# Optimization experiments

Hardware: AMD Instinct MI355X
Metric: run time of the kernel (lower is better)

## Reference

```python
import jax, jax.numpy as jnp
import numpy as np

N_NODES = 50000
N_EDGES = 1600000
IN_SIZE = 256
HIDDEN = 16
HEADS = 8
OUT_SIZE = 16
NEG_SLOPE = 0.2


def setup_inputs() -> dict:
    key = jax.random.key(0)
    ks = jax.random.split(key, 12)
    node_feat = jax.random.normal(ks[0], (N_NODES, IN_SIZE), dtype=jnp.float32)
    src = jax.random.randint(ks[1], (N_EDGES,), 0, N_NODES)
    dst = jax.random.randint(ks[2], (N_EDGES,), 0, N_NODES)
    d1 = HEADS * HIDDEN  # 128
    W1 = jax.random.normal(ks[3], (IN_SIZE, d1), dtype=jnp.float32) / np.sqrt(IN_SIZE)
    al1 = jax.random.normal(ks[4], (HEADS, HIDDEN), dtype=jnp.float32) / np.sqrt(HIDDEN)
    ar1 = jax.random.normal(ks[5], (HEADS, HIDDEN), dtype=jnp.float32) / np.sqrt(HIDDEN)
    b1 = jnp.zeros((d1,), dtype=jnp.float32)
    W2 = jax.random.normal(ks[6], (d1, HEADS * OUT_SIZE), dtype=jnp.float32) / np.sqrt(d1)
    al2 = jax.random.normal(ks[7], (HEADS, OUT_SIZE), dtype=jnp.float32) / np.sqrt(OUT_SIZE)
    ar2 = jax.random.normal(ks[8], (HEADS, OUT_SIZE), dtype=jnp.float32) / np.sqrt(OUT_SIZE)
    b2 = jnp.zeros((HEADS * OUT_SIZE,), dtype=jnp.float32)
    return {"node_feat": node_feat, "src": src, "dst": dst,
            "W1": W1, "al1": al1, "ar1": ar1, "b1": b1,
            "W2": W2, "al2": al2, "ar2": ar2, "b2": b2}


def _gat_conv(h, src, dst, W, attn_l, attn_r, bias, num_nodes):
    """DGL GATConv (eval mode, no dropout, no residual). Returns [N, H, D]."""
    H, D = attn_l.shape
    feat = (h @ W).reshape(-1, H, D)            # [N, H, D]
    el = jnp.sum(feat * attn_l, axis=-1)         # [N, H]
    er = jnp.sum(feat * attn_r, axis=-1)         # [N, H]
    e = jax.nn.leaky_relu(el[src] + er[dst], NEG_SLOPE)   # [E, H]
    # segment softmax over incoming edges of each dst node
    m = jax.ops.segment_max(e, dst, num_segments=num_nodes)
    m = jnp.where(jnp.isfinite(m), m, 0.0)       # guard isolated nodes
    ex = jnp.exp(e - m[dst])
    denom = jax.ops.segment_sum(ex, dst, num_segments=num_nodes)
    alpha = ex / denom[dst]                      # [E, H]
    msg = alpha[:, :, None] * feat[src]          # [E, H, D]
    out = jax.ops.segment_sum(msg, dst, num_segments=num_nodes)  # [N, H, D]
    return out + bias.reshape(H, D)


def reference(node_feat, src, dst, W1, al1, ar1, b1, W2, al2, ar2, b2):
    h = _gat_conv(node_feat, src, dst, W1, al1, ar1, b1, N_NODES)
    h = jax.nn.elu(h).reshape(N_NODES, -1)       # flatten(1) after activation
    out = _gat_conv(h, src, dst, W2, al2, ar2, b2, N_NODES)
    return out.mean(axis=1)                      # mean over heads -> [N, out_size]
```

## Files before the change

kernel.cpp:

```cpp
#include <hip/hip_runtime.h>
#include <hip/hip_bf16.h>

#define N_NODES 50000
#define N_EDGES 1600000
#define HEADS 8
#define HDIM 16
#define D1 128
#define NEG_SLOPE 0.2f
#define RTILES 3125
#define NB 196
#define BCAP 12288
#define B1BLK 320
#define EPB1 5000
#define WPREP_BLKS 217
#define GEMM_BLKS 782
#define B2BLK 392
#define B2CAP 8192

typedef short short8 __attribute__((ext_vector_type(8)));
typedef float f32x4 __attribute__((ext_vector_type(4)));
typedef _Float16 half8 __attribute__((ext_vector_type(8)));
typedef unsigned char uchar;

__device__ __forceinline__ float bf2f(ushort u) {
    union { unsigned u; float f; } x; x.u = ((unsigned)u) << 16; return x.f;
}
__device__ __forceinline__ ushort f2bf(float f) {
    union { float f; unsigned u; } x; x.f = f;
    unsigned r = x.u + 0x7FFF + ((x.u >> 16) & 1);
    return (ushort)(r >> 16);
}
__device__ __forceinline__ float ldf(const void* p, size_t i, int isf32) {
    return isf32 ? ((const float*)p)[i] : bf2f(((const ushort*)p)[i]);
}
__device__ __forceinline__ void splitbf(float f, ushort& hi, ushort& lo) {
    unsigned u = __float_as_uint(f);
    unsigned uh = u & 0xFFFF0000u;
    hi = (ushort)(uh >> 16);
    lo = f2bf(f - __uint_as_float(uh));
}

#define O_ROWPTR   0
#define O_GCUR     200064
#define O_FLAGS    602240
#define O_ESRC     2202624
#define O_W1HI     5402624
#define O_W1LO     5476352
#define O_W2HI     5550080
#define O_W2LO     5586944
#define O_B1F      5623808
#define O_B2F      5624320
#define O_FEATG    5624832
#define O_EL       18424832
#define O_ER       20024832
#define O_FEATG2   21624832
#define O_EL2      34424832
#define O_ER2      36024832
#define O_PKBUF    O_FEATG2


__global__ __launch_bounds__(256) void k_detect(const ushort* __restrict__ w1, int* __restrict__ flags,
                                                int* __restrict__ gcur) {
    __shared__ int sm[256];
    int t = threadIdx.x;
    if (blockIdx.x == 1) {
        if (t < NB) gcur[t] = 0;
        return;
    }
    int cnt = 0;
    for (int i = t; i < 32768; i += 256) {
        int e = (w1[i] >> 7) & 0xFF;
        if (e >= 0xC8) cnt++;
    }
    sm[t] = cnt; __syncthreads();
    for (int off = 128; off > 0; off >>= 1) {
        if (t < off) sm[t] += sm[t + off];
        __syncthreads();
    }
    if (t == 0) flags[0] = (sm[0] > 0) ? 1 : 0;
}

__device__ __forceinline__ void wprep_elem(const void* W, const void* al, const void* ar,
                                           int K, int kshift, ushort* whi, ushort* wlo,
                                           int isf32, int idx) {
    if (idx >= 144 * K) return;
    int n = idx >> kshift, k = idx & (K - 1);
    float f;
    if (n < 128) {
        f = ldf(W, (size_t)k * 128 + n, isf32);
    } else if (n < 136) {
        int h = n - 128;
        f = 0.f;
#pragma unroll
        for (int d = 0; d < HDIM; ++d)
            f = fmaf(ldf(W, (size_t)k * 128 + h * 16 + d, isf32), ldf(al, h * 16 + d, isf32), f);
    } else {
        int h = n - 136;
        f = 0.f;
#pragma unroll
        for (int d = 0; d < HDIM; ++d)
            f = fmaf(ldf(W, (size_t)k * 128 + h * 16 + d, isf32), ldf(ar, h * 16 + d, isf32), f);
    }
    ushort hi = f2bf(f);
    wlo[n * K + k] = f2bf(f - bf2f(hi));
    whi[n * K + k] = hi;
}

__device__ __forceinline__ void block_scan(int* sm, int t) {
    for (int off = 1; off < 256; off <<= 1) {
        int v = (t >= off) ? sm[t - off] : 0;
        __syncthreads();
        sm[t] += v;
        __syncthreads();
    }
}

#define B1_SMEM 28384

__global__ __launch_bounds__(256) void k_wb1(const void* __restrict__ W1, const void* __restrict__ al1,
                                             const void* __restrict__ ar1, const void* __restrict__ b1,
                                             const void* __restrict__ W2, const void* __restrict__ al2,
                                             const void* __restrict__ ar2, const void* __restrict__ b2,
                                             ushort* __restrict__ w1hi, ushort* __restrict__ w1lo,
                                             ushort* __restrict__ w2hi, ushort* __restrict__ w2lo,
                                             float* __restrict__ b1f, float* __restrict__ b2f,
                                             const int4* __restrict__ src4, const int4* __restrict__ dst4,
                                             int* __restrict__ gcur, uint* __restrict__ pkbuf,
                                             const int* __restrict__ flags) {
    __shared__ __align__(16) char smem[B1_SMEM];
    int b = blockIdx.x, t = threadIdx.x;
    if (b < WPREP_BLKS) {
        int isf32 = flags[0];
        if (b < 144) {
            wprep_elem(W1, al1, ar1, 256, 8, w1hi, w1lo, isf32, b * 256 + t);
        } else if (b < 216) {
            wprep_elem(W2, al2, ar2, 128, 7, w2hi, w2lo, isf32, (b - 144) * 256 + t);
        } else {
            if (t < 128) b1f[t] = ldf(b1, t, isf32);
            else b2f[t - 128] = ldf(b2, t - 128, isf32);
        }
    } else {
        uint*  stage = (uint*)smem;
        uchar* bid   = (uchar*)(smem + 20000);
        uint*  cnt   = (uint*)(smem + 25000);
        int*   loff  = (int*)(smem + 25784);
        int*   goff  = (int*)(smem + 26568);
        int*   sm    = (int*)(smem + 27352);
        int bb = b - WPREP_BLKS;
        for (int w = t; w < NB; w += 256) cnt[w] = 0;
        __syncthreads();
        int base4 = bb * (EPB1 / 4);
        for (int g = t; g < EPB1 / 4; g += 256) {
            int4 d = dst4[base4 + g];
            atomicAdd(&cnt[d.x >> 8], 1u);
            atomicAdd(&cnt[d.y >> 8], 1u);
            atomicAdd(&cnt[d.z >> 8], 1u);
            atomicAdd(&cnt[d.w >> 8], 1u);
        }
        __syncthreads();
        int c = (t < NB) ? (int)cnt[t] : 0;
        sm[t] = c;
        __syncthreads();
        block_scan(sm, t);
        if (t < NB) {
            loff[t] = sm[t] - c;
            goff[t] = atomicAdd(&gcur[t], c);
            cnt[t] = 0;
        }
        __syncthreads();
        for (int g = t; g < EPB1 / 4; g += 256) {
            int4 s = src4[base4 + g];
            int4 d = dst4[base4 + g];
            { int bk = d.x >> 8; int r = atomicAdd(&cnt[bk], 1u); int p = loff[bk] + r; stage[p] = ((uint)s.x << 8) | (uint)(d.x & 255); bid[p] = (uchar)bk; }
            { int bk = d.y >> 8; int r = atomicAdd(&cnt[bk], 1u); int p = loff[bk] + r; stage[p] = ((uint)s.y << 8) | (uint)(d.y & 255); bid[p] = (uchar)bk; }
            { int bk = d.z >> 8; int r = atomicAdd(&cnt[bk], 1u); int p = loff[bk] + r; stage[p] = ((uint)s.z << 8) | (uint)(d.z & 255); bid[p] = (uchar)bk; }
            { int bk = d.w >> 8; int r = atomicAdd(&cnt[bk], 1u); int p = loff[bk] + r; stage[p] = ((uint)s.w << 8) | (uint)(d.w & 255); bid[p] = (uchar)bk; }
        }
        __syncthreads();
        for (int k = t; k < EPB1; k += 256) {
            int bk = (int)bid[k];
            int gi = goff[bk] + (k - loff[bk]);
            if (gi < BCAP) pkbuf[(size_t)bk * BCAP + gi] = stage[k];
        }
    }
}

__device__ __forceinline__ void store_tile(_Float16 (*sfe)[72], _Float16* featg,
                                           const f32x4* acc, int lane, int quad, int l16,
                                           int rowb0, int cbase) {
#pragma unroll
    for (int ci = 0; ci < 4; ++ci)
#pragma unroll
        for (int r = 0; r < 4; ++r)
            sfe[quad * 4 + r][ci * 16 + l16] = (_Float16)acc[ci][r];
    int rr = lane >> 3, ch = lane & 7;
#pragma unroll
    for (int s = 0; s < 2; ++s) {
        int row = s * 8 + rr;
        short8 v = *(const short8*)&sfe[row][ch * 8];
        *(short8*)(featg + (size_t)(rowb0 + row) * D1 + cbase * 16 + ch * 8) = v;
    }
}

__device__ __forceinline__ void gemm1_wave9(const void* A, const ushort* Bhi, const ushort* Blo,
                                            _Float16* featg, float* el, float* er,
                                            int isf32, int rt, int lane, _Float16 (*sfe)[72]) {
    int quad = lane >> 4, l16 = lane & 15;
    const int K = 256;
    size_t a_off = (size_t)(rt * 16 + l16) * K + quad * 8;
    int rowb0 = rt * 16;

    short8 ahi[8], alo[8];
    if (isf32) {
        const float* ap = (const float*)A + a_off;
#pragma unroll
        for (int i = 0; i < 8; ++i) {
            f32x4 u0 = *(const f32x4*)(ap + 32 * i);
            f32x4 u1 = *(const f32x4*)(ap + 32 * i + 4);
            float a8[8] = {u0[0], u0[1], u0[2], u0[3], u1[0], u1[1], u1[2], u1[3]};
#pragma unroll
            for (int j = 0; j < 8; ++j) {
                ushort h, l;
                splitbf(a8[j], h, l);
                ahi[i][j] = (short)h; alo[i][j] = (short)l;
            }
        }
    } else {
        const ushort* ap = (const ushort*)A + a_off;
#pragma unroll
        for (int i = 0; i < 8; ++i) ahi[i] = *(const short8*)(ap + 32 * i);
    }

#pragma unroll
    for (int g = 0; g < 2; ++g) {
        f32x4 acc[4];
#pragma unroll
        for (int ci = 0; ci < 4; ++ci) acc[ci] = (f32x4){0.f, 0.f, 0.f, 0.f};
#pragma unroll
        for (int ci = 0; ci < 4; ++ci) {
            int c = g * 4 + ci;
            const ushort* bh = Bhi + (size_t)(c * 16 + l16) * K + quad * 8;
            if (isf32) {
                const ushort* bl = Blo + (size_t)(c * 16 + l16) * K + quad * 8;
#pragma unroll
                for (int k = 0; k < 8; ++k) {
                    short8 bh8 = *(const short8*)(bh + 32 * k);
                    short8 bl8 = *(const short8*)(bl + 32 * k);
                    acc[ci] = __builtin_amdgcn_mfma_f32_16x16x32_bf16(ahi[k], bh8, acc[ci], 0, 0, 0);
                    acc[ci] = __builtin_amdgcn_mfma_f32_16x16x32_bf16(ahi[k], bl8, acc[ci], 0, 0, 0);
                    acc[ci] = __builtin_amdgcn_mfma_f32_16x16x32_bf16(alo[k], bh8, acc[ci], 0, 0, 0);
                }
            } else {
#pragma unroll
                for (int k = 0; k < 8; ++k) {
                    short8 bh8 = *(const short8*)(bh + 32 * k);
                    acc[ci] = __builtin_amdgcn_mfma_f32_16x16x32_bf16(ahi[k], bh8, acc[ci], 0, 0, 0);
                }
            }
        }
        store_tile(sfe, featg, acc, lane, quad, l16, rowb0, g * 4);
    }

    {
        const ushort* bh = Bhi + (size_t)(8 * 16 + l16) * K + quad * 8;
        const ushort* bl = Blo + (size_t)(8 * 16 + l16) * K + quad * 8;
        f32x4 a = {0.f, 0.f, 0.f, 0.f};
#pragma unroll
        for (int k = 0; k < 8; ++k) {
            short8 bh8 = *(const short8*)(bh + 32 * k);
            short8 bl8 = *(const short8*)(bl + 32 * k);
            a = __builtin_amdgcn_mfma_f32_16x16x32_bf16(ahi[k], bh8, a, 0, 0, 0);
            a = __builtin_amdgcn_mfma_f32_16x16x32_bf16(ahi[k], bl8, a, 0, 0, 0);
            if (isf32) a = __builtin_amdgcn_mfma_f32_16x16x32_bf16(alo[k], bh8, a, 0, 0, 0);
        }
#pragma unroll
        for (int r = 0; r < 4; ++r) {
            int row = rowb0 + quad * 4 + r;
            if (l16 < 8) el[row * 8 + l16] = a[r];
            else         er[row * 8 + (l16 - 8)] = a[r];
        }
    }
}

#define G1B2_SMEM 19456

__global__ __launch_bounds__(256) void k_g1b2(const void* __restrict__ A,
                                              const ushort* __restrict__ w1hi, const ushort* __restrict__ w1lo,
                                              _Float16* __restrict__ featg,
                                              float* __restrict__ el, float* __restrict__ er,
                                              const uint* __restrict__ pkbuf, const int* __restrict__ gcur,
                                              ushort* __restrict__ esrc, int* __restrict__ rowptr,
                                              const int* __restrict__ flags) {
    __shared__ __align__(16) char smem[G1B2_SMEM];
    int b = blockIdx.x, t = threadIdx.x;
    if (b < GEMM_BLKS) {
        _Float16 (*sfe4)[16][72] = (_Float16(*)[16][72])smem;
        int wave = t >> 6, lane = t & 63;
        int rt = b * 4 + wave;
        if (rt < RTILES)
            gemm1_wave9(A, w1hi, w1lo, featg, el, er, flags[0], rt, lane, sfe4[wave]);
    } else {
        ushort* es    = (ushort*)smem;
        uint*   ncnt  = (uint*)(smem + 16384);
        int*    sm    = (int*)(smem + 17408);
        int*    nbase = (int*)(smem + 18432);
        int bb = b - GEMM_BLKS;
        int bk = bb >> 1, half = bb & 1;
        int x = (t < NB) ? gcur[t] : 0;
        sm[t] = x;
        __syncthreads();
        block_scan(sm, t);
        int nb = gcur[bk]; if (nb > BCAP) nb = BCAP;
        int bb0 = sm[bk] - gcur[bk];
        if (bb == 0 && t == NB - 1) rowptr[N_NODES] = sm[t];
        __syncthreads();
        ncnt[t] = 0;
        __syncthreads();
        const uint* pbase = pkbuf + (size_t)bk * BCAP;
        for (int k = t; k < nb; k += 256)
            atomicAdd(&ncnt[pbase[k] & 255u], 1u);
        __syncthreads();
        int c = (int)ncnt[t];
        sm[t] = c;
        __syncthreads();
        block_scan(sm, t);
        nbase[t] = sm[t] - c;
        int v = bk * 256 + t;
        if (v < N_NODES && (t >> 7) == half) rowptr[v] = bb0 + sm[t] - c;
        ncnt[t] = 0;
        __syncthreads();
        int lo = half * 128, hi = lo + 128;
        int base0 = nbase[lo];
        for (int k = t; k < nb; k += 256) {
            uint u = pbase[k];
            int n = (int)(u & 255u);
            if (n >= lo && n < hi) {
                int r = (int)atomicAdd(&ncnt[n], 1u);
                int p = nbase[n] + r - base0;
                if (p >= 0 && p < B2CAP) es[p] = (ushort)(u >> 8);
            }
        }
        __syncthreads();
        int myedges = sm[hi - 1] - base0;
        if (myedges > B2CAP) myedges = B2CAP;
        for (int k = t; k < myedges; k += 256)
            esrc[bb0 + base0 + k] = es[k];
    }
}

__device__ __forceinline__ void gather_wide(const int* __restrict__ rowptr, const ushort* __restrict__ esrc,
                                            const _Float16* __restrict__ featg,
                                            const float* __restrict__ el, const float* __restrict__ er,
                                            int v, int lane, float (&acc)[8], float& den, int& deg) {
    int h8 = lane & 7, esel = lane >> 3;
    int part = lane & 15, a = lane >> 4, hpart = part >> 1;
    float erv = er[v * 8 + h8];
    int beg = rowptr[v], end = rowptr[v + 1];
    deg = end - beg;
#pragma unroll
    for (int c = 0; c < 8; ++c) acc[c] = 0.f;
    den = 0.f;
    for (int j = beg; j < end; j += 8) {
        int nv = end - j;
        int idx = j + h8; if (idx >= end) idx = end - 1;
        int sv = (int)esrc[idx];
        int se = __shfl(sv, esel);
        float x = el[se * 8 + h8] + erv;
        x = x > 0.f ? x : NEG_SLOPE * x;
        float w = __expf(x);
        if (esel >= nv) w = 0.f;
        int s0 = __shfl(sv, a);
        int s1 = __shfl(sv, a + 4);
        half8 g0 = *(const half8*)(featg + (size_t)s0 * 128 + part * 8);
        half8 g1 = *(const half8*)(featg + (size_t)s1 * 128 + part * 8);
        float w0 = __shfl(w, a * 8 + hpart);
        float w1 = __shfl(w, (a + 4) * 8 + hpart);
        den += w0 + w1;
#pragma unroll
        for (int c = 0; c < 8; ++c)
            acc[c] = fmaf(w0, (float)g0[c], fmaf(w1, (float)g1[c], acc[c]));
    }
#pragma unroll
    for (int c = 0; c < 8; ++c) {
        acc[c] += __shfl_xor(acc[c], 16);
        acc[c] += __shfl_xor(acc[c], 32);
    }
    den += __shfl_xor(den, 16);
    den += __shfl_xor(den, 32);
}

__global__ __launch_bounds__(256) void k_agg1m(const int* __restrict__ rowptr, const ushort* __restrict__ esrc,
                                               const _Float16* __restrict__ featg,
                                               const float* __restrict__ el, const float* __restrict__ er,
                                               const float* __restrict__ b1f,
                                               const ushort* __restrict__ w2hi, const ushort* __restrict__ w2lo,
                                               _Float16* __restrict__ featg2,
                                               float* __restrict__ el2, float* __restrict__ er2,
                                               const int* __restrict__ flags, int boff) {
    __shared__ __align__(16) ushort sh_hi[16][136];
    __shared__ __align__(16) ushort sh_lo[16][136];
    int isf32 = flags[0];
    int wave = threadIdx.x >> 6, lane = threadIdx.x & 63;
    int part = lane & 15, a = lane >> 4;
    int vb = (blockIdx.x + boff) * 16;
    f32x4 bia0 = *(const f32x4*)(b1f + part * 8);
    f32x4 bia1 = *(const f32x4*)(b1f + part * 8 + 4);
#pragma unroll
    for (int i = 0; i < 4; ++i) {
        int v = vb + wave * 4 + i;
        float acc[8], den; int dg;
        gather_wide(rowptr, esrc, featg, el, er, v, lane, acc, den, dg);
        float inv = (dg > 0) ? 1.0f / den : 0.f;
        if (a == 0) {
            short8 hi8, lo8;
#pragma unroll
            for (int c = 0; c < 8; ++c) {
                float bc = (c < 4) ? bia0[c] : bia1[c - 4];
                float r = fmaf(acc[c], inv, bc);
                r = r > 0.f ? r : (__expf(r) - 1.f);
                ushort h, l;
                splitbf(r, h, l);
                hi8[c] = (short)h; lo8[c] = (short)l;
            }
            int m = wave * 4 + i;
            *(short8*)&sh_hi[m][part * 8] = hi8;
            *(short8*)&sh_lo[m][part * 8] = lo8;
        }
    }
    __syncthreads();

    int quad = lane >> 4, l16 = lane & 15;
    const int K = 128;
    short8 ahi[4], alo[4];
#pragma unroll
    for (int k = 0; k < 4; ++k) {
        ahi[k] = *(const short8*)&sh_hi[l16][quad * 8 + 32 * k];
        alo[k] = *(const short8*)&sh_lo[l16][quad * 8 + 32 * k];
    }
    int ntile = (wave == 0) ? 3 : 2;
    for (int ti = 0; ti < ntile; ++ti) {
        int c = (ti == 2) ? 8 : wave + ti * 4;
        const ushort* bh = w2hi + (size_t)(c * 16 + l16) * K + quad * 8;
        const ushort* bl = w2lo + (size_t)(c * 16 + l16) * K + quad * 8;
        f32x4 aa = {0.f, 0.f, 0.f, 0.f};
#pragma unroll
        for (int k = 0; k < 4; ++k) {
            short8 bh8 = *(const short8*)(bh + 32 * k);
            aa = __builtin_amdgcn_mfma_f32_16x16x32_bf16(ahi[k], bh8, aa, 0, 0, 0);
            aa = __builtin_amdgcn_mfma_f32_16x16x32_bf16(alo[k], bh8, aa, 0, 0, 0);
            if (c == 8 || isf32) {
                short8 bl8 = *(const short8*)(bl + 32 * k);
                aa = __builtin_amdgcn_mfma_f32_16x16x32_bf16(ahi[k], bl8, aa, 0, 0, 0);
            }
        }
        if (c < 8) {
#pragma unroll
            for (int r = 0; r < 4; ++r)
                featg2[(size_t)(vb + quad * 4 + r) * D1 + c * 16 + l16] = (_Float16)aa[r];
        } else {
#pragma unroll
            for (int r = 0; r < 4; ++r) {
                int row = vb + quad * 4 + r;
                if (l16 < 8) el2[row * 8 + l16] = aa[r];
                else         er2[row * 8 + (l16 - 8)] = aa[r];
            }
        }
    }
}

__global__ __launch_bounds__(256) void k_agg2(const int* __restrict__ rowptr, const ushort* __restrict__ esrc,
                                              const _Float16* __restrict__ featg2,
                                              const float* __restrict__ el2, const float* __restrict__ er2,
                                              const float* __restrict__ b2f,
                                              void* __restrict__ out, const int* __restrict__ flags, int boff) {
    int wave = threadIdx.x >> 6, lane = threadIdx.x & 63;
    int v = (blockIdx.x + boff) * 4 + wave;
    if (v >= N_NODES) return;
    int part = lane & 15;
    float acc[8], den; int dg;
    gather_wide(rowptr, esrc, featg2, el2, er2, v, lane, acc, den, dg);
    float inv = (dg > 0) ? 1.0f / den : 0.f;
    f32x4 bia0 = *(const f32x4*)(b2f + part * 8);
    f32x4 bia1 = *(const f32x4*)(b2f + part * 8 + 4);
    float r[8];
#pragma unroll
    for (int c = 0; c < 8; ++c) {
        float bc = (c < 4) ? bia0[c] : bia1[c - 4];
        r[c] = fmaf(acc[c], inv, bc);
    }
#pragma unroll
    for (int c = 0; c < 8; ++c) {
        r[c] += __shfl_xor(r[c], 2);
        r[c] += __shfl_xor(r[c], 4);
        r[c] += __shfl_xor(r[c], 8);
        r[c] *= 0.125f;
    }
    if (lane < 2) {
        if (flags[0]) {
            float* op = (float*)out + (size_t)v * 16 + lane * 8;
            f32x4 o0 = {r[0], r[1], r[2], r[3]};
            f32x4 o1 = {r[4], r[5], r[6], r[7]};
            *(f32x4*)op = o0;
            *(f32x4*)(op + 4) = o1;
        } else {
            short8 pk;
#pragma unroll
            for (int c = 0; c < 8; ++c) pk[c] = (short)f2bf(r[c]);
            *(short8*)((ushort*)out + (size_t)v * 16 + lane * 8) = pk;
        }
    }
}

extern "C" void kernel_launch(void* const* d_in, const int* in_sizes, int n_in,
                              void* d_out, int out_size, void* d_ws, size_t ws_size,
                              hipStream_t stream) {
    const void* node_feat = d_in[0];
    const int4* src4 = (const int4*)d_in[1];
    const int4* dst4 = (const int4*)d_in[2];
    const void* W1 = d_in[3];
    const void* al1 = d_in[4];
    const void* ar1 = d_in[5];
    const void* b1 = d_in[6];
    const void* W2 = d_in[7];
    const void* al2 = d_in[8];
    const void* ar2 = d_in[9];
    const void* b2 = d_in[10];
    char* ws = (char*)d_ws;

    int* rowptr = (int*)(ws + O_ROWPTR);
    int* gcur   = (int*)(ws + O_GCUR);
    int* flags  = (int*)(ws + O_FLAGS);
    ushort* esrc = (ushort*)(ws + O_ESRC);
    uint* pkbuf = (uint*)(ws + O_PKBUF);
    ushort* w1hi = (ushort*)(ws + O_W1HI);
    ushort* w1lo = (ushort*)(ws + O_W1LO);
    ushort* w2hi = (ushort*)(ws + O_W2HI);
    ushort* w2lo = (ushort*)(ws + O_W2LO);
    float* b1f  = (float*)(ws + O_B1F);
    float* b2f  = (float*)(ws + O_B2F);
    _Float16* featg = (_Float16*)(ws + O_FEATG);
    float* el   = (float*)(ws + O_EL);
    float* er   = (float*)(ws + O_ER);
    _Float16* featg2 = (_Float16*)(ws + O_FEATG2);
    float* el2  = (float*)(ws + O_EL2);
    float* er2  = (float*)(ws + O_ER2);

    k_detect<<<2, 256, 0, stream>>>((const ushort*)W1, flags, gcur);
    k_wb1<<<WPREP_BLKS + B1BLK, 256, 0, stream>>>(W1, al1, ar1, b1, W2, al2, ar2, b2,
                                                  w1hi, w1lo, w2hi, w2lo, b1f, b2f,
                                                  src4, dst4, gcur, pkbuf, flags);
    k_g1b2<<<GEMM_BLKS + B2BLK, 256, 0, stream>>>(node_feat, w1hi, w1lo, featg, el, er,
                                                  pkbuf, gcur, esrc, rowptr, flags);
    k_agg1m<<<1563, 256, 0, stream>>>(rowptr, esrc, featg, el, er, b1f,
                                      w2hi, w2lo, featg2, el2, er2, flags, 0);
    k_agg1m<<<1562, 256, 0, stream>>>(rowptr, esrc, featg, el, er, b1f,
                                      w2hi, w2lo, featg2, el2, er2, flags, 1563);
    k_agg2<<<6250, 256, 0, stream>>>(rowptr, esrc, featg2, el2, er2,
                                     b2f, d_out, flags, 0);
    k_agg2<<<6250, 256, 0, stream>>>(rowptr, esrc, featg2, el2, er2,
                                     b2f, d_out, flags, 6250);
}
```

Baseline: 393.2 us.

## Stage W1 tiles in LDS with double buffering for bf16 GEMM path

For bf16 inputs, the first-layer GEMM now stages each 16-row W1 slice in shared memory with an XOR swizzle and double buffering, so the four waves in a block share it instead of each reading B from global memory. The f32 path keeps direct global loads in a separate function. The split launches of the two aggregation kernels are also merged into single launches. This adds block-wide barriers and more LDS per block, and it only affects the bf16 path, which the harness may not exercise since the inputs are f32.

```diff
diff --git a/kernel.cpp b/kernel.cpp
--- a/kernel.cpp
+++ b/kernel.cpp
@@ -202,35 +202,104 @@
     }
 }
 
-__device__ __forceinline__ void gemm1_wave9(const void* A, const ushort* Bhi, const ushort* Blo,
-                                            _Float16* featg, float* el, float* er,
-                                            int isf32, int rt, int lane, _Float16 (*sfe)[72]) {
+__device__ __forceinline__ void stage_b(const ushort* __restrict__ src, int c,
+                                        ushort* __restrict__ dst , int t) {
+    int row = t >> 4, j = t & 15;
+    const ushort* s = src + (size_t)(c * 16 + row) * 256;
+    ushort* d = dst + row * 256;
+#pragma unroll
+    for (int h = 0; h < 2; ++h) {
+        int seg = 2 * j + h;
+        *(short8*)(d + (seg ^ row) * 8) = *(const short8*)(s + seg * 8);
+    }
+}
+
+__device__ __forceinline__ void gemm1_bf16_lds(const ushort* __restrict__ A,
+                                               const ushort* __restrict__ w1hi, const ushort* __restrict__ w1lo,
+                                               _Float16* featg, float* el, float* er,
+                                               int rt, int t, bool act,
+                                               ushort* __restrict__ Bb ,
+                                               _Float16 (*sfe)[72]) {
+    int lane = t & 63;
+    int quad = lane >> 4, l16 = lane & 15;
+    const int K = 256;
+    int rowb0 = rt * 16;
+    short8 ahi[8];
+    if (act) {
+        const ushort* ap = A + (size_t)(rowb0 + l16) * K + quad * 8;
+#pragma unroll
+        for (int i = 0; i < 8; ++i) ahi[i] = *(const short8*)(ap + 32 * i);
+    }
+    stage_b(w1hi, 0, Bb, t);
+    __syncthreads();
+    int cur = 0;
+#pragma unroll
+    for (int g = 0; g < 2; ++g) {
+        f32x4 acc[4];
+#pragma unroll
+        for (int ci = 0; ci < 4; ++ci) acc[ci] = (f32x4){0.f, 0.f, 0.f, 0.f};
+#pragma unroll
+        for (int ci = 0; ci < 4; ++ci) {
+            int c = g * 4 + ci;
+            stage_b(w1hi, c + 1, Bb + (cur ^ 1) * 4096, t);
+            if (act) {
+                const ushort* base = Bb + cur * 4096 + l16 * 256;
+#pragma unroll
+                for (int k = 0; k < 8; ++k) {
+                    int seg = quad + 4 * k;
+                    short8 bh8 = *(const short8*)(base + (seg ^ l16) * 8);
+                    acc[ci] = __builtin_amdgcn_mfma_f32_16x16x32_bf16(ahi[k], bh8, acc[ci], 0, 0, 0);
+                }
+            }
+            __syncthreads();
+            cur ^= 1;
+        }
+        if (act) store_tile(sfe, featg, acc, lane, quad, l16, rowb0, g * 4);
+    }
+    stage_b(w1lo, 8, Bb + (cur ^ 1) * 4096, t);
+    __syncthreads();
+    if (act) {
+        const ushort* bhb = Bb + cur * 4096 + l16 * 256;
+        const ushort* blb = Bb + (cur ^ 1) * 4096 + l16 * 256;
+        f32x4 a = {0.f, 0.f, 0.f, 0.f};
+#pragma unroll
+        for (int k = 0; k < 8; ++k) {
+            int seg = quad + 4 * k;
+            short8 bh8 = *(const short8*)(bhb + (seg ^ l16) * 8);
+            short8 bl8 = *(const short8*)(blb + (seg ^ l16) * 8);
+            a = __builtin_amdgcn_mfma_f32_16x16x32_bf16(ahi[k], bh8, a, 0, 0, 0);
+            a = __builtin_amdgcn_mfma_f32_16x16x32_bf16(ahi[k], bl8, a, 0, 0, 0);
+        }
+#pragma unroll
+        for (int r = 0; r < 4; ++r) {
+            int row = rowb0 + quad * 4 + r;
+            if (l16 < 8) el[row * 8 + l16] = a[r];
+            else         er[row * 8 + (l16 - 8)] = a[r];
+        }
+    }
+}
+
+__device__ __forceinline__ void gemm1_f32_direct(const void* A, const ushort* Bhi, const ushort* Blo,
+                                                 _Float16* featg, float* el, float* er,
+                                                 int rt, int lane, _Float16 (*sfe)[72]) {
     int quad = lane >> 4, l16 = lane & 15;
     const int K = 256;
     size_t a_off = (size_t)(rt * 16 + l16) * K + quad * 8;
     int rowb0 = rt * 16;
-
     short8 ahi[8], alo[8];
-    if (isf32) {
-        const float* ap = (const float*)A + a_off;
-#pragma unroll
-        for (int i = 0; i < 8; ++i) {
-            f32x4 u0 = *(const f32x4*)(ap + 32 * i);
-            f32x4 u1 = *(const f32x4*)(ap + 32 * i + 4);
-            float a8[8] = {u0[0], u0[1], u0[2], u0[3], u1[0], u1[1], u1[2], u1[3]};
-#pragma unroll
-            for (int j = 0; j < 8; ++j) {
-                ushort h, l;
-                splitbf(a8[j], h, l);
-                ahi[i][j] = (short)h; alo[i][j] = (short)l;
-            }
-        }
-    } else {
-        const ushort* ap = (const ushort*)A + a_off;
-#pragma unroll
-        for (int i = 0; i < 8; ++i) ahi[i] = *(const short8*)(ap + 32 * i);
-    }
-
+    const float* ap = (const float*)A + a_off;
+#pragma unroll
+    for (int i = 0; i < 8; ++i) {
+        f32x4 u0 = *(const f32x4*)(ap + 32 * i);
+        f32x4 u1 = *(const f32x4*)(ap + 32 * i + 4);
+        float a8[8] = {u0[0], u0[1], u0[2], u0[3], u1[0], u1[1], u1[2], u1[3]};
+#pragma unroll
+        for (int j = 0; j < 8; ++j) {
+            ushort h, l;
+            splitbf(a8[j], h, l);
+            ahi[i][j] = (short)h; alo[i][j] = (short)l;
+        }
+    }
 #pragma unroll
     for (int g = 0; g < 2; ++g) {
         f32x4 acc[4];
@@ -240,27 +309,18 @@
         for (int ci = 0; ci < 4; ++ci) {
             int c = g * 4 + ci;
             const ushort* bh = Bhi + (size_t)(c * 16 + l16) * K + quad * 8;
-            if (isf32) {
-                const ushort* bl = Blo + (size_t)(c * 16 + l16) * K + quad * 8;
-#pragma unroll
-                for (int k = 0; k < 8; ++k) {
-                    short8 bh8 = *(const short8*)(bh + 32 * k);
-                    short8 bl8 = *(const short8*)(bl + 32 * k);
-                    acc[ci] = __builtin_amdgcn_mfma_f32_16x16x32_bf16(ahi[k], bh8, acc[ci], 0, 0, 0);
-                    acc[ci] = __builtin_amdgcn_mfma_f32_16x16x32_bf16(ahi[k], bl8, acc[ci], 0, 0, 0);
-                    acc[ci] = __builtin_amdgcn_mfma_f32_16x16x32_bf16(alo[k], bh8, acc[ci], 0, 0, 0);
-                }
-            } else {
-#pragma unroll
-                for (int k = 0; k < 8; ++k) {
-                    short8 bh8 = *(const short8*)(bh + 32 * k);
-                    acc[ci] = __builtin_amdgcn_mfma_f32_16x16x32_bf16(ahi[k], bh8, acc[ci], 0, 0, 0);
-                }
+            const ushort* bl = Blo + (size_t)(c * 16 + l16) * K + quad * 8;
+#pragma unroll
+            for (int k = 0; k < 8; ++k) {
+                short8 bh8 = *(const short8*)(bh + 32 * k);
+                short8 bl8 = *(const short8*)(bl + 32 * k);
+                acc[ci] = __builtin_amdgcn_mfma_f32_16x16x32_bf16(ahi[k], bh8, acc[ci], 0, 0, 0);
+                acc[ci] = __builtin_amdgcn_mfma_f32_16x16x32_bf16(ahi[k], bl8, acc[ci], 0, 0, 0);
+                acc[ci] = __builtin_amdgcn_mfma_f32_16x16x32_bf16(alo[k], bh8, acc[ci], 0, 0, 0);
             }
         }
         store_tile(sfe, featg, acc, lane, quad, l16, rowb0, g * 4);
     }
-
     {
         const ushort* bh = Bhi + (size_t)(8 * 16 + l16) * K + quad * 8;
         const ushort* bl = Blo + (size_t)(8 * 16 + l16) * K + quad * 8;
@@ -271,7 +331,7 @@
             short8 bl8 = *(const short8*)(bl + 32 * k);
             a = __builtin_amdgcn_mfma_f32_16x16x32_bf16(ahi[k], bh8, a, 0, 0, 0);
             a = __builtin_amdgcn_mfma_f32_16x16x32_bf16(ahi[k], bl8, a, 0, 0, 0);
-            if (isf32) a = __builtin_amdgcn_mfma_f32_16x16x32_bf16(alo[k], bh8, a, 0, 0, 0);
+            a = __builtin_amdgcn_mfma_f32_16x16x32_bf16(alo[k], bh8, a, 0, 0, 0);
         }
 #pragma unroll
         for (int r = 0; r < 4; ++r) {
@@ -282,7 +342,7 @@
     }
 }
 
-#define G1B2_SMEM 19456
+#define G1B2_SMEM 25600
 
 __global__ __launch_bounds__(256) void k_g1b2(const void* __restrict__ A,
                                               const ushort* __restrict__ w1hi, const ushort* __restrict__ w1lo,
@@ -294,11 +354,18 @@
     __shared__ __align__(16) char smem[G1B2_SMEM];
     int b = blockIdx.x, t = threadIdx.x;
     if (b < GEMM_BLKS) {
-        _Float16 (*sfe4)[16][72] = (_Float16(*)[16][72])smem;
         int wave = t >> 6, lane = t & 63;
         int rt = b * 4 + wave;
-        if (rt < RTILES)
-            gemm1_wave9(A, w1hi, w1lo, featg, el, er, flags[0], rt, lane, sfe4[wave]);
+        if (flags[0]) {
+            _Float16 (*sfe4)[16][72] = (_Float16(*)[16][72])smem;
+            if (rt < RTILES)
+                gemm1_f32_direct(A, w1hi, w1lo, featg, el, er, rt, lane, sfe4[wave]);
+        } else {
+            ushort* Bb = (ushort*)smem;
+            _Float16 (*sfe4)[16][72] = (_Float16(*)[16][72])(smem + 16384);
+            gemm1_bf16_lds((const ushort*)A, w1hi, w1lo, featg, el, er,
+                           rt, t, rt < RTILES, Bb, sfe4[wave]);
+        }
     } else {
         ushort* es    = (ushort*)smem;
         uint*   ncnt  = (uint*)(smem + 16384);
@@ -396,13 +463,13 @@
                                                const ushort* __restrict__ w2hi, const ushort* __restrict__ w2lo,
                                                _Float16* __restrict__ featg2,
                                                float* __restrict__ el2, float* __restrict__ er2,
-                                               const int* __restrict__ flags, int boff) {
+                                               const int* __restrict__ flags) {
     __shared__ __align__(16) ushort sh_hi[16][136];
     __shared__ __align__(16) ushort sh_lo[16][136];
     int isf32 = flags[0];
     int wave = threadIdx.x >> 6, lane = threadIdx.x & 63;
     int part = lane & 15, a = lane >> 4;
-    int vb = (blockIdx.x + boff) * 16;
+    int vb = blockIdx.x * 16;
     f32x4 bia0 = *(const f32x4*)(b1f + part * 8);
     f32x4 bia1 = *(const f32x4*)(b1f + part * 8 + 4);
 #pragma unroll
@@ -472,9 +539,9 @@
                                               const _Float16* __restrict__ featg2,
                                               const float* __restrict__ el2, const float* __restrict__ er2,
                                               const float* __restrict__ b2f,
-                                              void* __restrict__ out, const int* __restrict__ flags, int boff) {
+                                              void* __restrict__ out, const int* __restrict__ flags) {
     int wave = threadIdx.x >> 6, lane = threadIdx.x & 63;
-    int v = (blockIdx.x + boff) * 4 + wave;
+    int v = blockIdx.x * 4 + wave;
     if (v >= N_NODES) return;
     int part = lane & 15;
     float acc[8], den; int dg;
@@ -551,12 +618,8 @@
                                                   src4, dst4, gcur, pkbuf, flags);
     k_g1b2<<<GEMM_BLKS + B2BLK, 256, 0, stream>>>(node_feat, w1hi, w1lo, featg, el, er,
                                                   pkbuf, gcur, esrc, rowptr, flags);
-    k_agg1m<<<1563, 256, 0, stream>>>(rowptr, esrc, featg, el, er, b1f,
-                                      w2hi, w2lo, featg2, el2, er2, flags, 0);
-    k_agg1m<<<1562, 256, 0, stream>>>(rowptr, esrc, featg, el, er, b1f,
-                                      w2hi, w2lo, featg2, el2, er2, flags, 1563);
-    k_agg2<<<6250, 256, 0, stream>>>(rowptr, esrc, featg2, el2, er2,
-                                     b2f, d_out, flags, 0);
-    k_agg2<<<6250, 256, 0, stream>>>(rowptr, esrc, featg2, el2, er2,
-                                     b2f, d_out, flags, 6250);
-}
+    k_agg1m<<<N_NODES / 16, 256, 0, stream>>>(rowptr, esrc, featg, el, er, b1f,
+                                              w2hi, w2lo, featg2, el2, er2, flags);
+    k_agg2<<<(N_NODES + 3) / 4, 256, 0, stream>>>(rowptr, esrc, featg2, el2, er2,
+                                                  b2f, d_out, flags);
+}
```

New measurement: 359.2 us. -8.6%, faster.
